# Performance work log

Measured on AMD Instinct MI355X. Metric: run time of the kernel, lower is better.

Reference implementation:

```python
import jax, jax.numpy as jnp
from jax import lax
import numpy as np

N, K, QK, W = 10, 10, 150, 128
D = 256
HID = 100
CHANS = [1, 16, 32, 64, 128, 256]
STRIDES = [2, 2, 1, 1, 1]
ITERS = 3
BN_EPS = 1e-5


def setup_inputs() -> dict:
    key = jax.random.key(0)
    ks = jax.random.split(key, 12)
    inp = {
        "support": jax.random.normal(ks[0], (N, K, 1, W, W), jnp.float32),
        "query": jax.random.normal(ks[1], (QK, 1, W, W), jnp.float32),
    }
    for i in range(5):
        inp[f"conv_w{i}"] = jax.random.normal(ks[2 + i], (CHANS[i + 1], CHANS[i], 3, 3), jnp.float32) * 0.05
        inp[f"bn_g{i}"] = jnp.ones((CHANS[i + 1],), jnp.float32)
        inp[f"bn_b{i}"] = jnp.zeros((CHANS[i + 1],), jnp.float32)
    inp["trans_w"] = jax.random.normal(ks[8], (D, D), jnp.float32) * 0.05
    inp["trans_b"] = jnp.zeros((D,), jnp.float32)
    inp["bil_w"] = jax.random.normal(ks[9], (HID, D, D), jnp.float32) * 0.02
    inp["score_w"] = jax.random.normal(ks[10], (1, HID), jnp.float32) * 0.1
    inp["score_b"] = jnp.zeros((1,), jnp.float32)
    return inp


def _block(x, w, g, b, s):
    # Conv2d(k=3, pad=1, stride=s, no bias) -> BatchNorm(eval: mean=0, var=1) -> ReLU -> MaxPool2d(2)
    x = lax.conv_general_dilated(x, w, (s, s), ((1, 1), (1, 1)),
                                 dimension_numbers=('NCHW', 'OIHW', 'NCHW'))
    scale = (g / jnp.sqrt(1.0 + BN_EPS))[None, :, None, None]
    x = jax.nn.relu(x * scale + b[None, :, None, None])
    return lax.reduce_window(x, -jnp.inf, lax.max, (1, 1, 2, 2), (1, 1, 2, 2), 'VALID')


def reference(support, query,
              conv_w0, conv_w1, conv_w2, conv_w3, conv_w4,
              bn_g0, bn_g1, bn_g2, bn_g3, bn_g4,
              bn_b0, bn_b1, bn_b2, bn_b3, bn_b4,
              trans_w, trans_b, bil_w, score_w, score_b):
    n, k = support.shape[0], support.shape[1]
    qk = query.shape[0]
    w = support.shape[3]

    ws = [conv_w0, conv_w1, conv_w2, conv_w3, conv_w4]
    gs = [bn_g0, bn_g1, bn_g2, bn_g3, bn_g4]
    bs = [bn_b0, bn_b1, bn_b2, bn_b3, bn_b4]

    # run the conv backbone on support+query jointly (BN is per-sample in eval mode)
    x = jnp.concatenate([support.reshape(n * k, 1, w, w), query], axis=0)
    for cw, g, b, s in zip(ws, gs, bs, STRIDES):
        x = _block(x, cw, g, b, s)
    feats = x.reshape(x.shape[0], -1)              # (n*k + qk, 256); spatial is 1x1
    sup = feats[:n * k].reshape(n, k, -1)          # (n, k, d)
    q = feats[n * k:]                              # (qk, d)

    # dynamic routing: Transformer(e) is recomputed each iter on the same input -> hoist
    e = sup @ trans_w.T + trans_b                  # (n, k, d)
    b0 = jnp.zeros((n, k), sup.dtype)

    def step(bb, _):
        dcoef = jax.nn.softmax(bb, axis=1)[:, :, None]   # (n, k, 1)
        c = (dcoef * e).sum(axis=1)                      # (n, d)
        cn = jnp.sqrt((c * c).sum(axis=1, keepdims=True))
        c = c * (cn / (cn * cn + 1.0))                   # squash: ||c||^2/(||c||^2+1)/||c||
        db = (c[:, None, :] * e).sum(axis=2)             # (n, k)
        return bb + db, c

    _, cs = lax.scan(step, b0, None, length=ITERS)
    proto = cs[-1]                                  # (n, d)

    # NTN: bilinear score for every (query, proto) pair, exploiting the pair structure
    t1 = jnp.einsum('nc,hce->nhe', proto, bil_w)    # (n, HID, d)
    v = jnp.einsum('nhe,qe->qnh', t1, q)            # (qk, n, HID)
    s = jax.nn.relu(v) @ score_w[0] + score_b[0]    # (qk, n)
    return jax.nn.log_softmax(s, axis=1)
```

## Files before the change

### kernel.cpp

```cpp
#include <hip/hip_runtime.h>
#include <math.h>


#define BN_SCALE rsqrtf(1.0f + 1e-5f)

#define OFF_FEATS 0
#define OFF_E     64000
#define OFF_S     89600
#define OFF_W1T   345600
#define OFF_W2T   350208
#define OFF_W3T   368640
#define OFF_W4T   442368
#define OFF_TWT   737280
#define OFF_PROTO 802816

__global__ void k_prep(const float* __restrict__ w1, const float* __restrict__ w2,
                       const float* __restrict__ w3, const float* __restrict__ w4,
                       const float* __restrict__ tw, float* __restrict__ ws) {
  float* w1t = ws + OFF_W1T;
  float* w2t = ws + OFF_W2T;
  float* w3t = ws + OFF_W3T;
  float* w4t = ws + OFF_W4T;
  float* twt = ws + OFF_TWT;
  int i = blockIdx.x * 256 + threadIdx.x;
  if (i < 4608) {
    int oc = i & 31; int r = i >> 5; int tap = r % 9; int ic = r / 9;
    w1t[i] = w1[(oc * 16 + ic) * 9 + tap];
  } else if (i < 23040) {
    int j = i - 4608;
    int oc = j & 63; int r = j >> 6; int tap = r % 9; int ic = r / 9;
    w2t[j] = w2[(oc * 32 + ic) * 9 + tap];
  } else if (i < 96768) {
    int j = i - 23040;
    int oc = j & 127; int r = j >> 7; int tap = r % 9; int ic = r / 9;
    w3t[j] = w3[(oc * 64 + ic) * 9 + tap];
  } else if (i < 391680) {
    int j = i - 96768;
    int oc = j & 255; int r = j >> 8; int tap = r % 9; int ic = r / 9;
    w4t[j] = w4[(oc * 128 + ic) * 9 + tap];
  } else {
    int j = i - 391680;
    int d = j >> 8, c = j & 255;
    twt[j] = tw[c * 256 + d];
  }
}

__global__ void __launch_bounds__(1024, 4)
k_main(const float* __restrict__ sup, const float* __restrict__ qry,
       const float* __restrict__ w0, const float* __restrict__ g0, const float* __restrict__ b0,
       const float* __restrict__ g1, const float* __restrict__ b1,
       const float* __restrict__ g2, const float* __restrict__ b2,
       const float* __restrict__ g3, const float* __restrict__ b3,
       const float* __restrict__ g4, const float* __restrict__ b4,
       const float* __restrict__ tb, float* __restrict__ ws,
       float* __restrict__ feats_g, float* __restrict__ e_buf) {
  __shared__ float S[28164];
  const float* w1t = ws + OFF_W1T;
  const float* w2t = ws + OFF_W2T;
  const float* w3t = ws + OFF_W3T;
  const float* w4t = ws + OFF_W4T;
  const float* twt = ws + OFF_TWT;
  const int img = blockIdx.x;
  const int t = threadIdx.x;
  const int lane = t & 63, wid = t >> 6;
  float* a0p = S + 8580;
  float* sa1 = S;
  float* sa2 = S + 4096;
  float* sa3 = S + 7424;
  float* sft = S + 7936;
  float* RED = S + 8580;

  const float* in = (img < 100) ? (sup + (size_t)img * 16384)
                                : (qry + (size_t)(img - 100) * 16384);

  {
    int oc = wid;
    float wv[9];
#pragma unroll
    for (int k = 0; k < 9; k++) wv[k] = w0[oc * 9 + k];
    float sc = g0[oc] * BN_SCALE, bs = b0[oc];
    int pcol = lane & 31, prh = lane >> 5;

    for (int i = t; i < 19584; i += 1024) a0p[i] = 0.f;

    for (int pass = 0; pass < 2; pass++) {
      __syncthreads();
      for (int i = t; i < 8580; i += 1024) {
        int r = i / 132, c = i % 132;
        int ir = pass ? (63 + r) : (r - 1);
        int icl = c - 1;
        S[i] = (ir >= 0 && ir < 128 && icl >= 0 && icl < 128) ? in[ir * 128 + icl] : 0.f;
      }
      __syncthreads();
#pragma unroll
      for (int it = 0; it < 8; it++) {
        int prl = it * 2 + prh;
        float win[25];
#pragma unroll
        for (int d = 0; d < 5; d++) {
          const float* rp = S + (4 * prl + d) * 132 + 4 * pcol;
          float4 r4 = *(const float4*)rp;
          win[d * 5 + 0] = r4.x; win[d * 5 + 1] = r4.y;
          win[d * 5 + 2] = r4.z; win[d * 5 + 3] = r4.w;
          win[d * 5 + 4] = rp[4];
        }
        float m = -1e30f;
#pragma unroll
        for (int a = 0; a < 2; a++)
#pragma unroll
          for (int b = 0; b < 2; b++) {
            float c = 0.f;
#pragma unroll
            for (int ky = 0; ky < 3; ky++)
#pragma unroll
              for (int kx = 0; kx < 3; kx++)
                c = fmaf(win[(2 * a + ky) * 5 + (2 * b + kx)], wv[ky * 3 + kx], c);
            m = fmaxf(m, fmaf(c, sc, bs));
          }
        int PR = pass * 16 + prl;
        a0p[oc * 1224 + (PR + 1) * 36 + (pcol + 1)] = fmaxf(m, 0.f);
      }
    }
  }
  __syncthreads();
  for (int i = t; i < 7424; i += 1024) S[i] = 0.f;
  __syncthreads();

  {
    int ocp = t & 15, pos = t >> 4;
    int py = pos >> 3, px = pos & 7;
    float acc0[4] = {0.f, 0.f, 0.f, 0.f}, acc1[4] = {0.f, 0.f, 0.f, 0.f};
    float2 wc[9];
#pragma unroll
    for (int k = 0; k < 9; k++) wc[k] = *(const float2*)(w1t + k * 32 + 2 * ocp);
    for (int ic = 0; ic < 16; ic++) {
      float2 wn[9];
      if (ic < 15) {
#pragma unroll
        for (int k = 0; k < 9; k++)
          wn[k] = *(const float2*)(w1t + ((ic + 1) * 9 + k) * 32 + 2 * ocp);
      }
      float win[25];
      const float* bp = a0p + ic * 1224 + 4 * py * 36 + 4 * px;
#pragma unroll
      for (int d = 0; d < 5; d++) {
        float4 r4 = *(const float4*)(bp + d * 36);
        win[d * 5 + 0] = r4.x; win[d * 5 + 1] = r4.y;
        win[d * 5 + 2] = r4.z; win[d * 5 + 3] = r4.w;
        win[d * 5 + 4] = bp[d * 36 + 4];
      }
#pragma unroll
      for (int cy = 0; cy < 2; cy++)
#pragma unroll
        for (int cx = 0; cx < 2; cx++) {
          float c0 = acc0[cy * 2 + cx], c1 = acc1[cy * 2 + cx];
#pragma unroll
          for (int ky = 0; ky < 3; ky++)
#pragma unroll
            for (int kx = 0; kx < 3; kx++) {
              float iv = win[(2 * cy + ky) * 5 + (2 * cx + kx)];
              c0 = fmaf(iv, wc[ky * 3 + kx].x, c0);
              c1 = fmaf(iv, wc[ky * 3 + kx].y, c1);
            }
          acc0[cy * 2 + cx] = c0; acc1[cy * 2 + cx] = c1;
        }
      if (ic < 15) {
#pragma unroll
        for (int k = 0; k < 9; k++) wc[k] = wn[k];
      }
    }
#pragma unroll
    for (int j = 0; j < 2; j++) {
      int oc = 2 * ocp + j;
      const float* ac = j ? acc1 : acc0;
      float sc = g1[oc] * BN_SCALE, bsj = b1[oc];
      float m = -1e30f;
#pragma unroll
      for (int p = 0; p < 4; p++) m = fmaxf(m, fmaf(ac[p], sc, bsj));
      sa1[oc * 124 + (py + 1) * 12 + (px + 1)] = fmaxf(m, 0.f);
    }
  }
  __syncthreads();

  {
    int oc = t & 63, icg = (t >> 6) & 3, pg = t >> 8;
    int pgy = pg >> 1, pgx = pg & 1;
    float acc[16];
#pragma unroll
    for (int p = 0; p < 16; p++) acc[p] = 0.f;
    float wc[9];
    {
      const float* wp = w2t + (icg * 8) * 576 + oc;
#pragma unroll
      for (int k = 0; k < 9; k++) wc[k] = wp[k * 64];
    }
    for (int ii = 0; ii < 8; ii++) {
      int ic = icg * 8 + ii;
      float wn[9];
      if (ii < 7) {
        const float* wp = w2t + (ic + 1) * 576 + oc;
#pragma unroll
        for (int k = 0; k < 9; k++) wn[k] = wp[k * 64];
      }
      float win[6][6];
      const float* bp = sa1 + ic * 124 + 4 * pgy * 12 + 4 * pgx;
#pragma unroll
      for (int d = 0; d < 6; d++) {
        float4 u = *(const float4*)(bp + d * 12);
        float2 v = *(const float2*)(bp + d * 12 + 4);
        win[d][0] = u.x; win[d][1] = u.y; win[d][2] = u.z; win[d][3] = u.w;
        win[d][4] = v.x; win[d][5] = v.y;
      }
#pragma unroll
      for (int u = 0; u < 4; u++)
#pragma unroll
        for (int v = 0; v < 4; v++) {
          float c = acc[u * 4 + v];
#pragma unroll
          for (int ky = 0; ky < 3; ky++)
#pragma unroll
            for (int kx = 0; kx < 3; kx++)
              c = fmaf(win[u + ky][v + kx], wc[ky * 3 + kx], c);
          acc[u * 4 + v] = c;
        }
      if (ii < 7) {
#pragma unroll
        for (int k = 0; k < 9; k++) wc[k] = wn[k];
      }
    }
#pragma unroll
    for (int j = 0; j < 16; j++) RED[j * 1024 + icg * 256 + pg * 64 + oc] = acc[j];
  }
  __syncthreads();
  if (t < 256) {
    int oc = t & 63, pg = t >> 6;
    int pgy = pg >> 1, pgx = pg & 1;
    float sc = g2[oc] * BN_SCALE, bsj = b2[oc];
#pragma unroll
    for (int cy = 0; cy < 2; cy++)
#pragma unroll
      for (int cx = 0; cx < 2; cx++) {
        float m = -1e30f;
#pragma unroll
        for (int a = 0; a < 2; a++)
#pragma unroll
          for (int b = 0; b < 2; b++) {
            int j = (2 * cy + a) * 4 + (2 * cx + b);
            float v = RED[j * 1024 + pg * 64 + oc] + RED[j * 1024 + 256 + pg * 64 + oc]
                    + RED[j * 1024 + 512 + pg * 64 + oc] + RED[j * 1024 + 768 + pg * 64 + oc];
            m = fmaxf(m, fmaf(v, sc, bsj));
          }
        sa2[oc * 52 + (1 + 2 * pgy + cy) * 8 + (1 + 2 * pgx + cx)] = fmaxf(m, 0.f);
      }
  }
  __syncthreads();

  {
    int oc = t & 127, icg = t >> 7;
    float acc[16];
#pragma unroll
    for (int p = 0; p < 16; p++) acc[p] = 0.f;
    float wc[9];
    {
      const float* wp = w3t + (icg * 8) * 1152 + oc;
#pragma unroll
      for (int k = 0; k < 9; k++) wc[k] = wp[k * 128];
    }
    for (int ii = 0; ii < 8; ii++) {
      int ic = icg * 8 + ii;
      float wn[9];
      if (ii < 7) {
        const float* wp = w3t + (ic + 1) * 1152 + oc;
#pragma unroll
        for (int k = 0; k < 9; k++) wn[k] = wp[k * 128];
      }
      float win[6][6];
      const float* bp = sa2 + ic * 52;
#pragma unroll
      for (int d = 0; d < 6; d++) {
        float4 u = *(const float4*)(bp + d * 8);
        float2 v = *(const float2*)(bp + d * 8 + 4);
        win[d][0] = u.x; win[d][1] = u.y; win[d][2] = u.z; win[d][3] = u.w;
        win[d][4] = v.x; win[d][5] = v.y;
      }
#pragma unroll
      for (int u = 0; u < 4; u++)
#pragma unroll
        for (int v = 0; v < 4; v++) {
          float c = acc[u * 4 + v];
#pragma unroll
          for (int ky = 0; ky < 3; ky++)
#pragma unroll
            for (int kx = 0; kx < 3; kx++)
              c = fmaf(win[u + ky][v + kx], wc[ky * 3 + kx], c);
          acc[u * 4 + v] = c;
        }
      if (ii < 7) {
#pragma unroll
        for (int k = 0; k < 9; k++) wc[k] = wn[k];
      }
    }
#pragma unroll
    for (int j = 0; j < 16; j++) RED[j * 1024 + icg * 128 + oc] = acc[j];
  }
  __syncthreads();
  if (t < 512) {
    int oc = t & 127, pp = t >> 7;
    int py = pp >> 1, px = pp & 1;
    float sc = g3[oc] * BN_SCALE, bsj = b3[oc];
    float m = -1e30f;
#pragma unroll
    for (int a = 0; a < 2; a++)
#pragma unroll
      for (int b = 0; b < 2; b++) {
        int j = (2 * py + a) * 4 + (2 * px + b);
        float v = 0.f;
#pragma unroll
        for (int g = 0; g < 8; g++) v += RED[j * 1024 + g * 128 + oc];
        m = fmaxf(m, fmaf(v, sc, bsj));
      }
    sa3[oc * 4 + pp] = fmaxf(m, 0.f);
  }
  __syncthreads();

  {
    int oc = t & 255, icq = t >> 8;
    float acc[4] = {0.f, 0.f, 0.f, 0.f};
    float wc[9];
    {
      const float* wp = w4t + (icq * 32) * 2304 + oc;
#pragma unroll
      for (int k = 0; k < 9; k++) wc[k] = wp[k * 256];
    }
    for (int ii = 0; ii < 32; ii++) {
      int ic = icq * 32 + ii;
      float wn[9];
      if (ii < 31) {
        const float* wp = w4t + (ic + 1) * 2304 + oc;
#pragma unroll
        for (int k = 0; k < 9; k++) wn[k] = wp[k * 256];
      }
      float4 iv = *(const float4*)(sa3 + ic * 4);
#pragma unroll
      for (int py = 0; py < 2; py++)
#pragma unroll
        for (int px = 0; px < 2; px++) {
          float c = acc[py * 2 + px];
          c = fmaf(iv.x, wc[(1 - py) * 3 + (1 - px)], c);
          c = fmaf(iv.y, wc[(1 - py) * 3 + (2 - px)], c);
          c = fmaf(iv.z, wc[(2 - py) * 3 + (1 - px)], c);
          c = fmaf(iv.w, wc[(2 - py) * 3 + (2 - px)], c);
          acc[py * 2 + px] = c;
        }
      if (ii < 31) {
#pragma unroll
        for (int k = 0; k < 9; k++) wc[k] = wn[k];
      }
    }
    if (icq) {
#pragma unroll
      for (int p = 0; p < 4; p++) RED[((icq - 1) * 256 + oc) * 4 + p] = acc[p];
    }
    __syncthreads();
    if (icq == 0) {
      float sc = g4[oc] * BN_SCALE, bsj = b4[oc];
      float m = -1e30f;
#pragma unroll
      for (int p = 0; p < 4; p++) {
        float v = acc[p] + RED[oc * 4 + p] + RED[(256 + oc) * 4 + p] + RED[(512 + oc) * 4 + p];
        m = fmaxf(m, fmaf(v, sc, bsj));
      }
      float r = fmaxf(m, 0.f);
      sft[oc] = r;
      feats_g[(size_t)img * 256 + oc] = r;
    }
  }
  __syncthreads();

  if (img < 100) {
    int c = t & 255, dq = t >> 8;
    float acc = 0.f;
    float wv = twt[(dq * 64) * 256 + c];
#pragma unroll 4
    for (int ii = 0; ii < 64; ii++) {
      int d = dq * 64 + ii;
      float wnext = (ii < 63) ? twt[(d + 1) * 256 + c] : 0.f;
      acc = fmaf(sft[d], wv, acc);
      wv = wnext;
    }
    if (dq) RED[(dq - 1) * 256 + c] = acc;
    __syncthreads();
    if (dq == 0)
      e_buf[img * 256 + c] = acc + RED[c] + RED[256 + c] + RED[512 + c] + tb[c];
  }
}

__global__ void k_routing(const float* __restrict__ e, float* __restrict__ proto,
                          float* __restrict__ s) {
  int n = blockIdx.x;
  __shared__ float sb[10], sdc[10], red[4], red2[40], sfc[1];
  int t = threadIdx.x;
  int lane = t & 63, wid = t >> 6;
  if (t < 150) s[n * 150 + t] = 0.f;
  float ek[10];
#pragma unroll
  for (int k = 0; k < 10; k++) ek[k] = e[n * 2560 + k * 256 + t];
  if (t < 10) sb[t] = 0.f;
  __syncthreads();
  float cd = 0.f;
  for (int iter = 0; iter < 3; iter++) {
    if (t == 0) {
      float mx = sb[0];
      for (int k = 1; k < 10; k++) mx = fmaxf(mx, sb[k]);
      float sum = 0.f;
      for (int k = 0; k < 10; k++) { float ex = expf(sb[k] - mx); sdc[k] = ex; sum += ex; }
      float inv = 1.f / sum;
      for (int k = 0; k < 10; k++) sdc[k] *= inv;
    }
    __syncthreads();
    cd = 0.f;
#pragma unroll
    for (int k = 0; k < 10; k++) cd = fmaf(sdc[k], ek[k], cd);
    float ss = cd * cd;
#pragma unroll
    for (int off = 32; off > 0; off >>= 1) ss += __shfl_down(ss, off, 64);
    if (lane == 0) red[wid] = ss;
    __syncthreads();
    if (t == 0) {
      float tot = red[0] + red[1] + red[2] + red[3];
      sfc[0] = sqrtf(tot) / (tot + 1.f);
    }
    __syncthreads();
    cd *= sfc[0];
    float pr[10];
#pragma unroll
    for (int k = 0; k < 10; k++) pr[k] = cd * ek[k];
#pragma unroll
    for (int off = 32; off > 0; off >>= 1)
#pragma unroll
      for (int k = 0; k < 10; k++) pr[k] += __shfl_down(pr[k], off, 64);
    if (lane == 0)
#pragma unroll
      for (int k = 0; k < 10; k++) red2[k * 4 + wid] = pr[k];
    __syncthreads();
    if (t < 10) sb[t] += red2[t * 4] + red2[t * 4 + 1] + red2[t * 4 + 2] + red2[t * 4 + 3];
    __syncthreads();
  }
  proto[n * 256 + t] = cd;
}

__global__ void k_hscore(const float* __restrict__ proto, const float* __restrict__ bw,
                         const float* __restrict__ qf, const float* __restrict__ sw,
                         float* __restrict__ s) {
  __shared__ float pt[3072];
  __shared__ float t1L[2600];
  __shared__ float qc[13000];
  const int h = blockIdx.x;
  const int t = threadIdx.x;
  for (int i = t; i < 2560; i += 256) {
    int n = i >> 8, c = i & 255;
    pt[c * 12 + n] = proto[i];
  }
  __syncthreads();
  {
    float acc[10];
#pragma unroll
    for (int n = 0; n < 10; n++) acc[n] = 0.f;
    const float* wp = bw + (size_t)h * 65536 + t;
#pragma unroll 2
    for (int c = 0; c < 256; c++) {
      float wv = wp[(size_t)c * 256];
      float4 p0 = *(const float4*)(pt + c * 12);
      float4 p1 = *(const float4*)(pt + c * 12 + 4);
      float2 p2 = *(const float2*)(pt + c * 12 + 8);
      acc[0] = fmaf(p0.x, wv, acc[0]); acc[1] = fmaf(p0.y, wv, acc[1]);
      acc[2] = fmaf(p0.z, wv, acc[2]); acc[3] = fmaf(p0.w, wv, acc[3]);
      acc[4] = fmaf(p1.x, wv, acc[4]); acc[5] = fmaf(p1.y, wv, acc[5]);
      acc[6] = fmaf(p1.z, wv, acc[6]); acc[7] = fmaf(p1.w, wv, acc[7]);
      acc[8] = fmaf(p2.x, wv, acc[8]); acc[9] = fmaf(p2.y, wv, acc[9]);
    }
#pragma unroll
    for (int n = 0; n < 10; n++) t1L[n * 260 + t] = acc[n];
  }
  float swh = sw[h];
  for (int ch = 0; ch < 3; ch++) {
    __syncthreads();
    int q0 = ch * 50;
    for (int i = t; i < 12800; i += 256) {
      int ql = i >> 8, e = i & 255;
      qc[ql * 260 + e] = qf[(q0 + ql) * 256 + e];
    }
    __syncthreads();
#pragma unroll
    for (int rep = 0; rep < 2; rep++) {
      int p = rep * 256 + t;
      if (p < 500) {
        int ql = p / 10, n = p % 10;
        const float4* tr = (const float4*)(t1L + n * 260);
        const float4* qr = (const float4*)(qc + ql * 260);
        float acc = 0.f;
#pragma unroll 4
        for (int d = 0; d < 64; d++) {
          float4 a = tr[d], b = qr[d];
          acc += a.x * b.x + a.y * b.y + a.z * b.z + a.w * b.w;
        }
        atomicAdd(&s[(q0 + ql) * 10 + n], fmaxf(acc, 0.f) * swh);
      }
    }
  }
}

__global__ void k_lsm(const float* __restrict__ s, const float* __restrict__ sbp,
                      float* __restrict__ out) {
  int q = threadIdx.x;
  if (q >= 150) return;
  float sb0 = sbp[0];
  float v[10];
  float mx = -1e30f;
#pragma unroll
  for (int n = 0; n < 10; n++) {
    v[n] = s[q * 10 + n] + sb0;
    mx = fmaxf(mx, v[n]);
  }
  float sum = 0.f;
#pragma unroll
  for (int n = 0; n < 10; n++) sum += expf(v[n] - mx);
  float lse = mx + logf(sum);
#pragma unroll
  for (int n = 0; n < 10; n++) out[q * 10 + n] = v[n] - lse;
}

extern "C" void kernel_launch(void* const* d_in, const int* in_sizes, int n_in,
                              void* d_out, int out_size, void* d_ws, size_t ws_size,
                              hipStream_t stream) {
  const float* support = (const float*)d_in[0];
  const float* query   = (const float*)d_in[1];
  const float* conv_w[5]; const float* bn_g[5]; const float* bn_b[5];
  for (int i = 0; i < 5; i++) {
    conv_w[i] = (const float*)d_in[2 + 3 * i];
    bn_g[i]   = (const float*)d_in[3 + 3 * i];
    bn_b[i]   = (const float*)d_in[4 + 3 * i];
  }
  const float* trans_w = (const float*)d_in[17];
  const float* trans_b = (const float*)d_in[18];
  const float* bil_w   = (const float*)d_in[19];
  const float* score_w = (const float*)d_in[20];
  const float* score_b = (const float*)d_in[21];
  float* out = (float*)d_out;
  float* ws = (float*)d_ws;

  float* feats = ws + OFF_FEATS;
  float* e_buf = ws + OFF_E;
  float* s_buf = ws + OFF_S;
  float* proto = ws + OFF_PROTO;

  k_prep<<<1786, 256, 0, stream>>>(conv_w[1], conv_w[2], conv_w[3], conv_w[4],
                                   trans_w, ws);
  k_main<<<250, 1024, 0, stream>>>(support, query,
                                   conv_w[0], bn_g[0], bn_b[0],
                                   bn_g[1], bn_b[1], bn_g[2], bn_b[2],
                                   bn_g[3], bn_b[3], bn_g[4], bn_b[4],
                                   trans_b, ws, feats, e_buf);
  k_routing<<<10, 256, 0, stream>>>(e_buf, proto, s_buf);
  k_hscore<<<100, 256, 0, stream>>>(proto, bil_w, feats + 100 * 256,
                                    score_w, s_buf);
  k_lsm<<<1, 256, 0, stream>>>(s_buf, score_b, out);
}
```

Measured before the change: 256.2 us.

## Split bilinear scoring into split-K t1 kernel and per-query score kernel

Replaces the 100-block k_hscore with two kernels. k_t1 spreads the proto×bil_w contraction over 800 blocks (split over c in chunks of 32) and accumulates into a global t1 buffer with atomics. k_score then computes query·t1 dot products per (query, half of HID), applies relu and score weights, and atomically adds into s. Zeroing of t1 and s moves into k_prep. This aims to fill the GPU better in the NTN stage, at the cost of an extra launch, float atomics and a round trip of t1 through global memory.

```diff
diff --git a/kernel.cpp b/kernel.cpp
--- a/kernel.cpp
+++ b/kernel.cpp
@@ -7,12 +7,13 @@
 #define OFF_FEATS 0
 #define OFF_E     64000
 #define OFF_S     89600
-#define OFF_W1T   345600
-#define OFF_W2T   350208
-#define OFF_W3T   368640
-#define OFF_W4T   442368
-#define OFF_TWT   737280
-#define OFF_PROTO 802816
+#define OFF_T1    91136
+#define OFF_PROTO 347136
+#define OFF_W1T   349696
+#define OFF_W2T   354304
+#define OFF_W3T   372736
+#define OFF_W4T   446464
+#define OFF_TWT   741376
 
 __global__ void k_prep(const float* __restrict__ w1, const float* __restrict__ w2,
                        const float* __restrict__ w3, const float* __restrict__ w4,
@@ -38,10 +39,14 @@
     int j = i - 96768;
     int oc = j & 255; int r = j >> 8; int tap = r % 9; int ic = r / 9;
     w4t[j] = w4[(oc * 128 + ic) * 9 + tap];
-  } else {
+  } else if (i < 457216) {
     int j = i - 391680;
     int d = j >> 8, c = j & 255;
     twt[j] = tw[c * 256 + d];
+  } else if (i < 713216) {
+    ws[OFF_T1 + (i - 457216)] = 0.f;
+  } else if (i < 714716) {
+    ws[OFF_S + (i - 713216)] = 0.f;
   }
 }
 
@@ -395,13 +400,11 @@
   }
 }
 
-__global__ void k_routing(const float* __restrict__ e, float* __restrict__ proto,
-                          float* __restrict__ s) {
+__global__ void k_routing(const float* __restrict__ e, float* __restrict__ proto) {
   int n = blockIdx.x;
   __shared__ float sb[10], sdc[10], red[4], red2[40], sfc[1];
   int t = threadIdx.x;
   int lane = t & 63, wid = t >> 6;
-  if (t < 150) s[n * 150 + t] = 0.f;
   float ek[10];
 #pragma unroll
   for (int k = 0; k < 10; k++) ek[k] = e[n * 2560 + k * 256 + t];
@@ -449,64 +452,73 @@
   proto[n * 256 + t] = cd;
 }
 
-__global__ void k_hscore(const float* __restrict__ proto, const float* __restrict__ bw,
-                         const float* __restrict__ qf, const float* __restrict__ sw,
-                         float* __restrict__ s) {
-  __shared__ float pt[3072];
-  __shared__ float t1L[2600];
-  __shared__ float qc[13000];
-  const int h = blockIdx.x;
+__global__ void k_t1(const float* __restrict__ proto, const float* __restrict__ bw,
+                     float* __restrict__ t1) {
+  __shared__ float pt[384];
+  const int b = blockIdx.x;
+  const int h = b >> 3, c0 = (b & 7) * 32;
   const int t = threadIdx.x;
-  for (int i = t; i < 2560; i += 256) {
-    int n = i >> 8, c = i & 255;
-    pt[c * 12 + n] = proto[i];
-  }
-  __syncthreads();
-  {
-    float acc[10];
-#pragma unroll
-    for (int n = 0; n < 10; n++) acc[n] = 0.f;
-    const float* wp = bw + (size_t)h * 65536 + t;
-#pragma unroll 2
-    for (int c = 0; c < 256; c++) {
-      float wv = wp[(size_t)c * 256];
-      float4 p0 = *(const float4*)(pt + c * 12);
-      float4 p1 = *(const float4*)(pt + c * 12 + 4);
-      float2 p2 = *(const float2*)(pt + c * 12 + 8);
-      acc[0] = fmaf(p0.x, wv, acc[0]); acc[1] = fmaf(p0.y, wv, acc[1]);
-      acc[2] = fmaf(p0.z, wv, acc[2]); acc[3] = fmaf(p0.w, wv, acc[3]);
-      acc[4] = fmaf(p1.x, wv, acc[4]); acc[5] = fmaf(p1.y, wv, acc[5]);
-      acc[6] = fmaf(p1.z, wv, acc[6]); acc[7] = fmaf(p1.w, wv, acc[7]);
-      acc[8] = fmaf(p2.x, wv, acc[8]); acc[9] = fmaf(p2.y, wv, acc[9]);
-    }
-#pragma unroll
-    for (int n = 0; n < 10; n++) t1L[n * 260 + t] = acc[n];
-  }
-  float swh = sw[h];
-  for (int ch = 0; ch < 3; ch++) {
-    __syncthreads();
-    int q0 = ch * 50;
-    for (int i = t; i < 12800; i += 256) {
-      int ql = i >> 8, e = i & 255;
-      qc[ql * 260 + e] = qf[(q0 + ql) * 256 + e];
-    }
-    __syncthreads();
-#pragma unroll
-    for (int rep = 0; rep < 2; rep++) {
-      int p = rep * 256 + t;
-      if (p < 500) {
-        int ql = p / 10, n = p % 10;
-        const float4* tr = (const float4*)(t1L + n * 260);
-        const float4* qr = (const float4*)(qc + ql * 260);
-        float acc = 0.f;
+  for (int i = t; i < 320; i += 256) {
+    int n = i >> 5, cl = i & 31;
+    pt[cl * 12 + n] = proto[n * 256 + c0 + cl];
+  }
+  __syncthreads();
+  float acc[10];
+#pragma unroll
+  for (int n = 0; n < 10; n++) acc[n] = 0.f;
+  const float* wp = bw + (size_t)h * 65536 + (size_t)c0 * 256 + t;
 #pragma unroll 4
-        for (int d = 0; d < 64; d++) {
-          float4 a = tr[d], b = qr[d];
-          acc += a.x * b.x + a.y * b.y + a.z * b.z + a.w * b.w;
-        }
-        atomicAdd(&s[(q0 + ql) * 10 + n], fmaxf(acc, 0.f) * swh);
-      }
-    }
+  for (int cl = 0; cl < 32; cl++) {
+    float wv = wp[(size_t)cl * 256];
+    float4 p0 = *(const float4*)(pt + cl * 12);
+    float4 p1 = *(const float4*)(pt + cl * 12 + 4);
+    float2 p2 = *(const float2*)(pt + cl * 12 + 8);
+    acc[0] = fmaf(p0.x, wv, acc[0]); acc[1] = fmaf(p0.y, wv, acc[1]);
+    acc[2] = fmaf(p0.z, wv, acc[2]); acc[3] = fmaf(p0.w, wv, acc[3]);
+    acc[4] = fmaf(p1.x, wv, acc[4]); acc[5] = fmaf(p1.y, wv, acc[5]);
+    acc[6] = fmaf(p1.z, wv, acc[6]); acc[7] = fmaf(p1.w, wv, acc[7]);
+    acc[8] = fmaf(p2.x, wv, acc[8]); acc[9] = fmaf(p2.y, wv, acc[9]);
+  }
+#pragma unroll
+  for (int n = 0; n < 10; n++)
+    atomicAdd(&t1[((size_t)n * 100 + h) * 256 + t], acc[n]);
+}
+
+__global__ void k_score(const float* __restrict__ t1, const float* __restrict__ qf,
+                        const float* __restrict__ sw, float* __restrict__ s) {
+  __shared__ float sq[256];
+  __shared__ float vb[2000];
+  const int q = blockIdx.x >> 1, hh = blockIdx.x & 1;
+  const int t = threadIdx.x;
+  const int sl = t & 3, quad = t >> 2;
+  sq[t] = qf[q * 256 + t];
+  __syncthreads();
+  const float4* qr = (const float4*)sq;
+#pragma unroll
+  for (int j = 0; j < 8; j++) {
+    int lr = quad + 64 * j;
+    if (lr < 500) {
+      int n = lr / 50, hl = lr % 50;
+      const float4* row = (const float4*)(t1 + ((size_t)(n * 100 + hh * 50 + hl)) * 256);
+      float acc = 0.f;
+#pragma unroll
+      for (int d = 0; d < 16; d++) {
+        float4 a = row[d * 4 + sl];
+        float4 b = qr[d * 4 + sl];
+        acc += a.x * b.x + a.y * b.y + a.z * b.z + a.w * b.w;
+      }
+      vb[lr * 4 + sl] = acc;
+    }
+  }
+  __syncthreads();
+  if (t < 10) {
+    float sum = 0.f;
+    for (int hl = 0; hl < 50; hl++) {
+      int lr = t * 50 + hl;
+      float d = vb[lr * 4] + vb[lr * 4 + 1] + vb[lr * 4 + 2] + vb[lr * 4 + 3];
+      sum = fmaf(fmaxf(d, 0.f), sw[hh * 50 + hl], sum);
+    }
+    atomicAdd(&s[q * 10 + t], sum);
   }
 }
 
@@ -552,17 +564,18 @@
   float* feats = ws + OFF_FEATS;
   float* e_buf = ws + OFF_E;
   float* s_buf = ws + OFF_S;
+  float* t1    = ws + OFF_T1;
   float* proto = ws + OFF_PROTO;
 
-  k_prep<<<1786, 256, 0, stream>>>(conv_w[1], conv_w[2], conv_w[3], conv_w[4],
+  k_prep<<<2793, 256, 0, stream>>>(conv_w[1], conv_w[2], conv_w[3], conv_w[4],
                                    trans_w, ws);
   k_main<<<250, 1024, 0, stream>>>(support, query,
                                    conv_w[0], bn_g[0], bn_b[0],
                                    bn_g[1], bn_b[1], bn_g[2], bn_b[2],
                                    bn_g[3], bn_b[3], bn_g[4], bn_b[4],
                                    trans_b, ws, feats, e_buf);
-  k_routing<<<10, 256, 0, stream>>>(e_buf, proto, s_buf);
-  k_hscore<<<100, 256, 0, stream>>>(proto, bil_w, feats + 100 * 256,
-                                    score_w, s_buf);
+  k_routing<<<10, 256, 0, stream>>>(e_buf, proto);
+  k_t1<<<800, 256, 0, stream>>>(proto, bil_w, t1);
+  k_score<<<300, 256, 0, stream>>>(t1, feats + 100 * 256, score_w, s_buf);
   k_lsm<<<1, 256, 0, stream>>>(s_buf, score_b, out);
 }
```

Result: faster. 215.9 us (-15.7%).
